# Performance work log

Hardware: AMD Instinct MI355X
Metric: run time of the kernel (lower is better)

Reference implementation:

```python
import jax, jax.numpy as jnp
import numpy as np

B, NT, NM, C, H, FF = 8, 1024, 2048, 1024, 8, 4096


def setup_inputs() -> dict:
    key = jax.random.key(0)
    ks = jax.random.split(key, 8)
    w = lambda k, shape, s=0.02: jax.random.normal(k, shape, dtype=jnp.float32) * s
    return {
        "tgt": jax.random.normal(ks[0], (B, NT, C), dtype=jnp.float32),
        "memory": jax.random.normal(ks[1], (B, NM, C), dtype=jnp.float32),
        "qkv_w": w(ks[2], (3 * C, C)), "qkv_b": jnp.zeros((3 * C,), jnp.float32),
        "sa_out_w": w(ks[3], (C, C)), "sa_out_b": jnp.zeros((C,), jnp.float32),
        "in_proj_w": w(ks[4], (3 * C, C)), "in_proj_b": jnp.zeros((3 * C,), jnp.float32),
        "mha_out_w": w(ks[5], (C, C)), "mha_out_b": jnp.zeros((C,), jnp.float32),
        "lin1_w": w(ks[6], (FF, C)), "lin1_b": jnp.zeros((FF,), jnp.float32),
        "lin2_w": w(ks[7], (C, FF)), "lin2_b": jnp.zeros((C,), jnp.float32),
        "ln1_g": jnp.ones((C,), jnp.float32), "ln1_b": jnp.zeros((C,), jnp.float32),
        "ln2_g": jnp.ones((C,), jnp.float32), "ln2_b": jnp.zeros((C,), jnp.float32),
        "ln3_g": jnp.ones((C,), jnp.float32), "ln3_b": jnp.zeros((C,), jnp.float32),
    }


def _ln(x, g, b):
    m = x.mean(-1, keepdims=True)
    v = jnp.mean((x - m) ** 2, axis=-1, keepdims=True)
    return (x - m) / jnp.sqrt(v + 1e-5) * g + b


def reference(tgt, memory, qkv_w, qkv_b, sa_out_w, sa_out_b,
              in_proj_w, in_proj_b, mha_out_w, mha_out_b,
              lin1_w, lin1_b, lin2_w, lin2_b,
              ln1_g, ln1_b, ln2_g, ln2_b, ln3_g, ln3_b):
    Bx, N, Cx = tgt.shape
    # ---- LocalSelfAttention: dense QK^T masked to diagonal-only window ----
    qkv = tgt @ qkv_w.T + qkv_b                      # [B,N,3C]
    q, k, v = jnp.split(qkv, 3, axis=-1)             # each [B,N,C]
    # NOTE: original multiplies by sqrt(embed_dim) (scale = sqrt, not 1/sqrt)
    scores = jnp.einsum('bnc,bmc->bnm', q, k) * jnp.sqrt(jnp.float32(Cx))
    diag = jnp.eye(N, dtype=bool)                    # registered diagonal mask
    scores = jnp.where(diag[None, :, :], scores, -jnp.inf)
    attn = jax.nn.softmax(scores, axis=-1)           # degenerates to identity
    sa = jnp.einsum('bnm,bmc->bnc', attn, v) @ sa_out_w.T + sa_out_b
    x = _ln(tgt + sa, ln1_g, ln1_b)
    # ---- cross multi-head attention over memory ----
    d = Cx // H
    wq, wk, wv = jnp.split(in_proj_w, 3, axis=0)
    bq, bk, bv = jnp.split(in_proj_b, 3, axis=0)
    qh = (x @ wq.T + bq).reshape(Bx, N, H, d).transpose(0, 2, 1, 3)       # [B,H,N,d]
    kh = (memory @ wk.T + bk).reshape(Bx, -1, H, d).transpose(0, 2, 1, 3)  # [B,H,M,d]
    vh = (memory @ wv.T + bv).reshape(Bx, -1, H, d).transpose(0, 2, 1, 3)
    a = jax.nn.softmax(jnp.einsum('bhnd,bhmd->bhnm', qh, kh) / jnp.sqrt(jnp.float32(d)), axis=-1)
    ca = jnp.einsum('bhnm,bhmd->bhnd', a, vh).transpose(0, 2, 1, 3).reshape(Bx, N, Cx)
    ca = ca @ mha_out_w.T + mha_out_b
    x = _ln(x + ca, ln2_g, ln2_b)
    # ---- FFN (relu) ----
    ff = jax.nn.relu(x @ lin1_w.T + lin1_b) @ lin2_w.T + lin2_b
    return _ln(x + ff, ln3_g, ln3_b)
```

## Files before the change

kernel.cpp:

```cpp
#include <hip/hip_runtime.h>
#include <hip/hip_bf16.h>
#include <cstddef>
#include <cstdint>

static constexpr int Cdim = 1024;
static constexpr int Bdim = 8;
static constexpr int NT   = 1024;
static constexpr int NM   = 2048;
static constexpr int Dh   = 128;
static constexpr int FF   = 4096;

typedef __attribute__((ext_vector_type(8))) short bf16x8_t;
typedef __attribute__((ext_vector_type(4))) float f32x4_t;

__device__ __forceinline__ float bf2f(unsigned int u16) {
    return __uint_as_float(u16 << 16);
}
__device__ __forceinline__ unsigned short f2bf(float f) {
    unsigned int u = __float_as_uint(f);
    u += 0x7fffu + ((u >> 16) & 1u);
    return (unsigned short)(u >> 16);
}

__device__ __forceinline__ void gload16(const void* g, void* l) {
    __builtin_amdgcn_global_load_lds(
        (const __attribute__((address_space(1))) void*)g,
        (__attribute__((address_space(3))) void*)l, 16, 0, 0);
}

__global__ __launch_bounds__(256)
void cvt_k(const float* __restrict__ in, unsigned short* __restrict__ out, int n8)
{
    const int stride = gridDim.x * 256;
    for (int i = blockIdx.x * 256 + threadIdx.x; i < n8; i += stride) {
        const float4 a = ((const float4*)in)[2*i];
        const float4 b = ((const float4*)in)[2*i+1];
        uint4 o;
        o.x = (unsigned)f2bf(a.x) | ((unsigned)f2bf(a.y) << 16);
        o.y = (unsigned)f2bf(a.z) | ((unsigned)f2bf(a.w) << 16);
        o.z = (unsigned)f2bf(b.x) | ((unsigned)f2bf(b.y) << 16);
        o.w = (unsigned)f2bf(b.z) | ((unsigned)f2bf(b.w) << 16);
        ((uint4*)out)[i] = o;
    }
}

template<int EPI, bool OBF>
__global__ __launch_bounds__(256)
void gemm_bf16_k(const unsigned short* __restrict__ A,
                 const unsigned short* __restrict__ W,
                 const float* __restrict__ bias, const float* __restrict__ resid,
                 void* __restrict__ outv, int Rows, int Cout, int K)
{
    __shared__ unsigned short As[128*32];
    __shared__ unsigned short Bs[128*32];
    const int gx  = gridDim.x;
    const int lin = blockIdx.y * gx + blockIdx.x;
    const int cpx = (gx * gridDim.y) >> 3;
    const int swz = (lin & 7) * cpx + (lin >> 3);
    const int bm = (swz / gx) * 128;
    const int bn = (swz % gx) * 128;
    const int t = threadIdx.x;
    const int w = t >> 6, l = t & 63;
    const int wr = w >> 1, wc = w & 1;

    f32x4_t acc[4][4];
    #pragma unroll
    for (int m = 0; m < 4; ++m)
        #pragma unroll
        for (int n = 0; n < 4; ++n) acc[m][n] = {0.f, 0.f, 0.f, 0.f};

    const int rA = 2*w*16 + (l >> 2);
    const int kc = (l & 3) * 8;
    const unsigned short* gA0 = A + (size_t)(bm + rA) * K + kc;
    const unsigned short* gA1 = gA0 + (size_t)16 * K;
    const unsigned short* gB0 = W + (size_t)(bn + rA) * K + kc;
    const unsigned short* gB1 = gB0 + (size_t)16 * K;
    unsigned short* lA0 = As + 2*w*512;
    unsigned short* lA1 = As + (2*w+1)*512;
    unsigned short* lB0 = Bs + 2*w*512;
    unsigned short* lB1 = Bs + (2*w+1)*512;

    const int frow = l & 15;
    const int kq   = l >> 4;
    const int abase = (wr*64 + frow)*64 + kq*16;
    const int bbase = (wc*64 + frow)*64 + kq*16;

    for (int k0 = 0; k0 < K; k0 += 32) {
        gload16(gA0, lA0); gload16(gA1, lA1);
        gload16(gB0, lB0); gload16(gB1, lB1);
        gA0 += 32; gA1 += 32; gB0 += 32; gB1 += 32;
        __syncthreads();
        bf16x8_t af[4], bfr[4];
        #pragma unroll
        for (int m = 0; m < 4; ++m)
            af[m] = *(const bf16x8_t*)((const char*)As + abase + m*1024);
        #pragma unroll
        for (int n = 0; n < 4; ++n)
            bfr[n] = *(const bf16x8_t*)((const char*)Bs + bbase + n*1024);
        #pragma unroll
        for (int m = 0; m < 4; ++m)
            #pragma unroll
            for (int n = 0; n < 4; ++n)
                acc[m][n] = __builtin_amdgcn_mfma_f32_16x16x32_bf16(
                                af[m], bfr[n], acc[m][n], 0, 0, 0);
        __syncthreads();
    }

    const int col0 = l & 15;
    const int r0   = (l >> 4) * 4;
    float bv[4];
    #pragma unroll
    for (int n = 0; n < 4; ++n) bv[n] = bias[bn + wc*64 + n*16 + col0];

    #pragma unroll
    for (int m = 0; m < 4; ++m)
        #pragma unroll
        for (int r = 0; r < 4; ++r) {
            const int row = bm + wr*64 + m*16 + r0 + r;
            #pragma unroll
            for (int n = 0; n < 4; ++n) {
                const int col = bn + wc*64 + n*16 + col0;
                const size_t idx = (size_t)row * Cout + col;
                float v = acc[m][n][r] + bv[n];
                if (EPI == 1) v += resid[idx];
                if (EPI == 2) v = fmaxf(v, 0.f);
                if (OBF) ((unsigned short*)outv)[idx] = f2bf(v);
                else     ((float*)outv)[idx] = v;
            }
        }
}

__global__ __launch_bounds__(256)
void vtrans_k(const unsigned short* __restrict__ kvb, unsigned short* __restrict__ vT)
{
    __shared__ unsigned short Ls[64][80];
    const int mt = blockIdx.x;
    const int ct = blockIdx.y;
    const int b  = blockIdx.z;
    const int t  = threadIdx.x;
    const int lr = t >> 3;
    const int cc = (t & 7) * 8;
    #pragma unroll
    for (int i = 0; i < 2; ++i) {
        const int m = lr + i*32;
        const uint4 v = *(const uint4*)(kvb +
            ((size_t)(b*NM + mt*64 + m))*(2*Cdim) + Cdim + ct*64 + cc);
        const unsigned short* s = (const unsigned short*)&v;
        #pragma unroll
        for (int j = 0; j < 8; ++j) {
            const int row = cc + j;
            Ls[row][8*((m >> 3) ^ (row >> 3)) + (m & 7)] = s[j];
        }
    }
    __syncthreads();
    #pragma unroll
    for (int i = 0; i < 2; ++i) {
        const int c  = lr + i*32;
        const int cg = ct*64 + c;
        const int h  = cg >> 7, dd = cg & 127;
        const uint4 v = *(const uint4*)&Ls[c][8*((t & 7) ^ (c >> 3))];
        *(uint4*)(vT + ((size_t)((b*8 + h)*128 + dd))*NM + mt*64 + cc) = v;
    }
}

__global__ __launch_bounds__(256)
void flash_attn_k(const unsigned short* __restrict__ qh,
                  const unsigned short* __restrict__ kvb,
                  const unsigned short* __restrict__ vT,
                  unsigned short* __restrict__ ca)
{
    __shared__ unsigned short Ks [64*128];
    __shared__ unsigned short VTs[128*64];
    __shared__ unsigned short Ps [64*64];

    const int lin = blockIdx.y * 16 + blockIdx.x;
    const int swz = (lin & 7) * 128 + (lin >> 3);
    const int qt = swz & 15;
    const int bh = swz >> 4;
    const int b = bh >> 3, h = bh & 7;
    const int t = threadIdx.x;
    const int w = t >> 6, l = t & 63;
    const float scale = 0.08838834764831845f;

    bf16x8_t aq[4];
    {
        const unsigned short* qbase = qh +
            ((size_t)(b*NT + qt*64 + w*16 + (l & 15)))*Cdim + h*Dh + (l >> 4)*8;
        #pragma unroll
        for (int kk = 0; kk < 4; ++kk)
            aq[kk] = *(const bf16x8_t*)(qbase + kk*32);
    }

    const unsigned short* ksrc[4];
    const unsigned short* vsrc[4];
    #pragma unroll
    for (int j = 0; j < 4; ++j) {
        const int chunk = 4*w + j;
        const int krow  = chunk*4 + (l >> 4);
        ksrc[j] = kvb + (size_t)(b*NM + krow)*(2*Cdim) + h*Dh
                      + (((l & 15) ^ (krow & 7)) * 8);
        const int dd = chunk*8 + (l >> 3);
        vsrc[j] = vT + (size_t)(bh*128 + dd)*NM + (((l & 7) ^ (dd & 7)) * 8);
    }
    unsigned short* kdst = Ks  + 4*w*512;
    unsigned short* vdst = VTs + 4*w*512;

    f32x4_t oacc[8];
    #pragma unroll
    for (int n = 0; n < 8; ++n) oacc[n] = {0.f, 0.f, 0.f, 0.f};
    float mrow[4] = {-1e30f, -1e30f, -1e30f, -1e30f};
    float lsum[4] = {0.f, 0.f, 0.f, 0.f};

    for (int m0 = 0; m0 < NM; m0 += 64) {
        __syncthreads();
        #pragma unroll
        for (int j = 0; j < 4; ++j) {
            gload16(ksrc[j] + (size_t)m0*(2*Cdim), kdst + j*512);
            gload16(vsrc[j] + m0,                  vdst + j*512);
        }
        __syncthreads();

        f32x4_t sacc[4];
        #pragma unroll
        for (int n = 0; n < 4; ++n) sacc[n] = {0.f, 0.f, 0.f, 0.f};
        #pragma unroll
        for (int n = 0; n < 4; ++n) {
            const int key = 16*n + (l & 15);
            #pragma unroll
            for (int kk = 0; kk < 4; ++kk) {
                const int slot = 4*kk + (l >> 4);
                const bf16x8_t bk = *(const bf16x8_t*)
                    (Ks + key*128 + ((slot ^ (key & 7)) * 8));
                sacc[n] = __builtin_amdgcn_mfma_f32_16x16x32_bf16(
                              aq[kk], bk, sacc[n], 0, 0, 0);
            }
        }

        #pragma unroll
        for (int r = 0; r < 4; ++r) {
            float s0 = sacc[0][r]*scale, s1 = sacc[1][r]*scale;
            float s2 = sacc[2][r]*scale, s3 = sacc[3][r]*scale;
            float cm = fmaxf(fmaxf(s0, s1), fmaxf(s2, s3));
            cm = fmaxf(cm, __shfl_xor(cm, 1, 16));
            cm = fmaxf(cm, __shfl_xor(cm, 2, 16));
            cm = fmaxf(cm, __shfl_xor(cm, 4, 16));
            cm = fmaxf(cm, __shfl_xor(cm, 8, 16));
            const float mnew = fmaxf(mrow[r], cm);
            const float corr = __expf(mrow[r] - mnew);
            mrow[r] = mnew;
            const float p0 = __expf(s0 - mnew), p1 = __expf(s1 - mnew);
            const float p2 = __expf(s2 - mnew), p3 = __expf(s3 - mnew);
            float rs = p0 + p1 + p2 + p3;
            rs += __shfl_xor(rs, 1, 16);
            rs += __shfl_xor(rs, 2, 16);
            rs += __shfl_xor(rs, 4, 16);
            rs += __shfl_xor(rs, 8, 16);
            lsum[r] = lsum[r]*corr + rs;
            #pragma unroll
            for (int n = 0; n < 8; ++n) oacc[n][r] *= corr;
            const int q = w*16 + (l >> 4)*4 + r;
            const float pv[4] = {p0, p1, p2, p3};
            #pragma unroll
            for (int n = 0; n < 4; ++n) {
                const int k = 16*n + (l & 15);
                Ps[q*64 + (((k >> 3) ^ (q & 7)) * 8) + (k & 7)] = f2bf(pv[n]);
            }
        }

        #pragma unroll
        for (int kk = 0; kk < 2; ++kk) {
            const int qa   = w*16 + (l & 15);
            const int slot = 4*kk + (l >> 4);
            const bf16x8_t pa = *(const bf16x8_t*)
                (Ps + qa*64 + ((slot ^ (qa & 7)) * 8));
            #pragma unroll
            for (int n = 0; n < 8; ++n) {
                const int dd = 16*n + (l & 15);
                const bf16x8_t bv = *(const bf16x8_t*)
                    (VTs + dd*64 + ((slot ^ (dd & 7)) * 8));
                oacc[n] = __builtin_amdgcn_mfma_f32_16x16x32_bf16(
                              pa, bv, oacc[n], 0, 0, 0);
            }
        }
    }

    #pragma unroll
    for (int r = 0; r < 4; ++r) {
        const float rinv = 1.0f / lsum[r];
        unsigned short* crow = ca +
            ((size_t)(b*NT + qt*64 + w*16 + (l >> 4)*4 + r))*Cdim + h*Dh + (l & 15);
        #pragma unroll
        for (int n = 0; n < 8; ++n)
            crow[16*n] = f2bf(oacc[n][r] * rinv);
    }
}

template<bool DUAL>
__global__ __launch_bounds__(256)
void ln_k(const float* __restrict__ in, const float* __restrict__ gam,
          const float* __restrict__ bet, float* __restrict__ out,
          unsigned short* __restrict__ out_bf)
{
    __shared__ float red[8];
    const int row = blockIdx.x;
    const int t = threadIdx.x;
    const float4 x = *(const float4*)(in + (size_t)row*Cdim + t*4);
    float s = x.x + x.y + x.z + x.w;
    #pragma unroll
    for (int m = 1; m < 64; m <<= 1) s += __shfl_xor(s, m, 64);
    if ((t & 63) == 0) red[t >> 6] = s;
    __syncthreads();
    const float mean = (red[0]+red[1]+red[2]+red[3]) * (1.0f/1024.0f);
    const float dx = x.x-mean, dy = x.y-mean, dz = x.z-mean, dw = x.w-mean;
    float q = dx*dx + dy*dy + dz*dz + dw*dw;
    #pragma unroll
    for (int m = 1; m < 64; m <<= 1) q += __shfl_xor(q, m, 64);
    if ((t & 63) == 0) red[4 + (t >> 6)] = q;
    __syncthreads();
    const float var = (red[4]+red[5]+red[6]+red[7]) * (1.0f/1024.0f);
    const float inv = 1.0f / sqrtf(var + 1e-5f);
    const float4 g  = *(const float4*)(gam + t*4);
    const float4 bb = *(const float4*)(bet + t*4);
    const float r0 = dx*inv*g.x+bb.x, r1 = dy*inv*g.y+bb.y;
    const float r2 = dz*inv*g.z+bb.z, r3 = dw*inv*g.w+bb.w;
    *(float4*)(out + (size_t)row*Cdim + t*4) = make_float4(r0,r1,r2,r3);
    if (DUAL) {
        uint2 pk;
        pk.x = (unsigned)f2bf(r0) | ((unsigned)f2bf(r1) << 16);
        pk.y = (unsigned)f2bf(r2) | ((unsigned)f2bf(r3) << 16);
        *(uint2*)(out_bf + (size_t)row*Cdim + t*4) = pk;
    }
}

extern "C" void kernel_launch(void* const* d_in, const int* in_sizes, int n_in,
                              void* d_out, int out_size, void* d_ws, size_t ws_size,
                              hipStream_t stream)
{
    const float* tgt      = (const float*)d_in[0];
    const float* memory   = (const float*)d_in[1];
    const float* qkv_w    = (const float*)d_in[2];
    const float* qkv_b    = (const float*)d_in[3];
    const float* sa_out_w = (const float*)d_in[4];
    const float* sa_out_b = (const float*)d_in[5];
    const float* in_w     = (const float*)d_in[6];
    const float* in_b     = (const float*)d_in[7];
    const float* mha_w    = (const float*)d_in[8];
    const float* mha_b    = (const float*)d_in[9];
    const float* lin1_w   = (const float*)d_in[10];
    const float* lin1_b   = (const float*)d_in[11];
    const float* lin2_w   = (const float*)d_in[12];
    const float* lin2_b   = (const float*)d_in[13];
    const float* ln1_g    = (const float*)d_in[14];
    const float* ln1_bb   = (const float*)d_in[15];
    const float* ln2_g    = (const float*)d_in[16];
    const float* ln2_bb   = (const float*)d_in[17];
    const float* ln3_g    = (const float*)d_in[18];
    const float* ln3_bb   = (const float*)d_in[19];

    const size_t MB = 1024*1024;
    if (ws_size < 220*MB) return;
    char* p = (char*)d_ws;
    unsigned short* wv   = (unsigned short*)p; p += 2*MB;
    unsigned short* wsa  = (unsigned short*)p; p += 2*MB;
    unsigned short* win  = (unsigned short*)p; p += 6*MB;
    unsigned short* wmh  = (unsigned short*)p; p += 2*MB;
    unsigned short* wl1  = (unsigned short*)p; p += 8*MB;
    unsigned short* wl2  = (unsigned short*)p; p += 8*MB;
    float* resb = (float*)p; p += 32*MB;
    float* x12  = (float*)p; p += 32*MB;
    unsigned short* kvff = (unsigned short*)p; p += 64*MB;
    unsigned short* vq   = (unsigned short*)p; p += 16*MB;
    unsigned short* regG = (unsigned short*)p; p += 16*MB;
    unsigned short* regH = (unsigned short*)p; p += 32*MB;
    unsigned short* vT   = (unsigned short*)resb;
    unsigned short* tgtb = regG;
    unsigned short* x1b  = regG;
    unsigned short* memb = regH;
    unsigned short* cabf = regH;
    unsigned short* x2b  = (unsigned short*)((char*)regH + 16*MB);
    float* x1 = x12;
    float* x2 = x12;

    const int R  = Bdim * NT;
    const int RM = Bdim * NM;
    dim3 blk(256);
    auto cvgrid = [](int n8){ int b = (n8 + 255) / 256; return dim3(b > 2048 ? 2048 : b); };

    cvt_k<<<cvgrid(R*Cdim/8),      blk, 0, stream>>>(tgt,                 tgtb, R*Cdim/8);
    cvt_k<<<cvgrid(RM*Cdim/8),     blk, 0, stream>>>(memory,              memb, RM*Cdim/8);
    cvt_k<<<cvgrid(Cdim*Cdim/8),   blk, 0, stream>>>(qkv_w + 2*Cdim*Cdim, wv,   Cdim*Cdim/8);
    cvt_k<<<cvgrid(Cdim*Cdim/8),   blk, 0, stream>>>(sa_out_w,            wsa,  Cdim*Cdim/8);
    cvt_k<<<cvgrid(3*Cdim*Cdim/8), blk, 0, stream>>>(in_w,                win,  3*Cdim*Cdim/8);
    cvt_k<<<cvgrid(Cdim*Cdim/8),   blk, 0, stream>>>(mha_w,               wmh,  Cdim*Cdim/8);
    cvt_k<<<cvgrid(FF*Cdim/8),     blk, 0, stream>>>(lin1_w,              wl1,  FF*Cdim/8);
    cvt_k<<<cvgrid(FF*Cdim/8),     blk, 0, stream>>>(lin2_w,              wl2,  FF*Cdim/8);

    gemm_bf16_k<0,true ><<<dim3( 8,  64), blk, 0, stream>>>(tgtb, wv,  qkv_b + 2*Cdim, nullptr, vq,   R,  Cdim,   Cdim);
    gemm_bf16_k<1,false><<<dim3( 8,  64), blk, 0, stream>>>(vq,   wsa, sa_out_b,       tgt,     resb, R,  Cdim,   Cdim);
    ln_k<true ><<<dim3(R), blk, 0, stream>>>(resb, ln1_g, ln1_bb, x1, x1b);
    gemm_bf16_k<0,true ><<<dim3( 8,  64), blk, 0, stream>>>(x1b,  win, in_b,           nullptr, vq,   R,  Cdim,   Cdim);
    gemm_bf16_k<0,true ><<<dim3(16, 128), blk, 0, stream>>>(memb, win + Cdim*Cdim, in_b + Cdim, nullptr, kvff, RM, 2*Cdim, Cdim);
    vtrans_k<<<dim3(32, 16, 8), blk, 0, stream>>>(kvff, vT);
    flash_attn_k<<<dim3(16, 64), blk, 0, stream>>>(vq, kvff, vT, cabf);
    gemm_bf16_k<1,false><<<dim3( 8,  64), blk, 0, stream>>>(cabf, wmh, mha_b,          x1,      resb, R,  Cdim,   Cdim);
    ln_k<true ><<<dim3(R), blk, 0, stream>>>(resb, ln2_g, ln2_bb, x2, x2b);
    gemm_bf16_k<2,true ><<<dim3(32,  64), blk, 0, stream>>>(x2b,  wl1, lin1_b,         nullptr, kvff, R,  FF,     Cdim);
    gemm_bf16_k<1,false><<<dim3( 8,  64), blk, 0, stream>>>(kvff, wl2, lin2_b,         x2,      resb, R,  Cdim,   FF);
    ln_k<false><<<dim3(R), blk, 0, stream>>>(resb, ln3_g, ln3_bb, (float*)d_out, nullptr);
}
```

Baseline: 866.1 us.

## Double-buffer flash attention K/V loads, fuse conversions, wave-per-row layernorm

Flash attention now prefetches the next K/V tile into a second LDS buffer while computing on the current one, using explicit vmcnt waits, and raises wave priority around the MFMA sections. The eight fp32-to-bf16 conversion launches are merged into one kernel that picks its segment by block index. Layernorm is reorganized so each wavefront handles one row, dropping the shared-memory reduction and block barriers. Doubling LDS use in attention may lower occupancy.

```diff
diff --git a/kernel.cpp b/kernel.cpp
--- a/kernel.cpp
+++ b/kernel.cpp
@@ -28,20 +28,29 @@
         (__attribute__((address_space(3))) void*)l, 16, 0, 0);
 }
 
+struct CvtArgs {
+    const float* src[8];
+    unsigned short* dst[8];
+};
+
 __global__ __launch_bounds__(256)
-void cvt_k(const float* __restrict__ in, unsigned short* __restrict__ out, int n8)
-{
-    const int stride = gridDim.x * 256;
-    for (int i = blockIdx.x * 256 + threadIdx.x; i < n8; i += stride) {
-        const float4 a = ((const float4*)in)[2*i];
-        const float4 b = ((const float4*)in)[2*i+1];
-        uint4 o;
-        o.x = (unsigned)f2bf(a.x) | ((unsigned)f2bf(a.y) << 16);
-        o.y = (unsigned)f2bf(a.z) | ((unsigned)f2bf(a.w) << 16);
-        o.z = (unsigned)f2bf(b.x) | ((unsigned)f2bf(b.y) << 16);
-        o.w = (unsigned)f2bf(b.z) | ((unsigned)f2bf(b.w) << 16);
-        ((uint4*)out)[i] = o;
-    }
+void cvt_all_k(CvtArgs a)
+{
+    constexpr int cum[8] = {0, 8, 24, 25, 26, 29, 30, 34};
+    const int u = blockIdx.x >> 9;
+    int seg = 0;
+    #pragma unroll
+    for (int s = 1; s < 8; ++s) seg = (u >= cum[s]) ? s : seg;
+    const size_t i8 = (size_t)(blockIdx.x - (cum[seg] << 9)) * 256 + threadIdx.x;
+    const float* sp = a.src[seg] + i8 * 8;
+    const float4 x = ((const float4*)sp)[0];
+    const float4 y = ((const float4*)sp)[1];
+    uint4 o;
+    o.x = (unsigned)f2bf(x.x) | ((unsigned)f2bf(x.y) << 16);
+    o.y = (unsigned)f2bf(x.z) | ((unsigned)f2bf(x.w) << 16);
+    o.z = (unsigned)f2bf(y.x) | ((unsigned)f2bf(y.y) << 16);
+    o.w = (unsigned)f2bf(y.z) | ((unsigned)f2bf(y.w) << 16);
+    *(uint4*)(a.dst[seg] + i8 * 8) = o;
 }
 
 template<int EPI, bool OBF>
@@ -169,8 +178,8 @@
                   const unsigned short* __restrict__ vT,
                   unsigned short* __restrict__ ca)
 {
-    __shared__ unsigned short Ks [64*128];
-    __shared__ unsigned short VTs[128*64];
+    __shared__ unsigned short Ks [2][64*128];
+    __shared__ unsigned short VTs[2][128*64];
     __shared__ unsigned short Ps [64*64];
 
     const int lin = blockIdx.y * 16 + blockIdx.x;
@@ -202,8 +211,6 @@
         const int dd = chunk*8 + (l >> 3);
         vsrc[j] = vT + (size_t)(bh*128 + dd)*NM + (((l & 7) ^ (dd & 7)) * 8);
     }
-    unsigned short* kdst = Ks  + 4*w*512;
-    unsigned short* vdst = VTs + 4*w*512;
 
     f32x4_t oacc[8];
     #pragma unroll
@@ -211,18 +218,33 @@
     float mrow[4] = {-1e30f, -1e30f, -1e30f, -1e30f};
     float lsum[4] = {0.f, 0.f, 0.f, 0.f};
 
-    for (int m0 = 0; m0 < NM; m0 += 64) {
-        __syncthreads();
-        #pragma unroll
-        for (int j = 0; j < 4; ++j) {
-            gload16(ksrc[j] + (size_t)m0*(2*Cdim), kdst + j*512);
-            gload16(vsrc[j] + m0,                  vdst + j*512);
-        }
-        __syncthreads();
+    #pragma unroll
+    for (int j = 0; j < 4; ++j) {
+        gload16(ksrc[j], &Ks[0][4*w*512 + j*512]);
+        gload16(vsrc[j], &VTs[0][4*w*512 + j*512]);
+    }
+
+    for (int tt = 0; tt < 32; ++tt) {
+        const int buf = tt & 1;
+        if (tt < 31) {
+            const size_t koff = (size_t)((tt + 1) * 64) * (2*Cdim);
+            const int    moff = (tt + 1) * 64;
+            #pragma unroll
+            for (int j = 0; j < 4; ++j) {
+                gload16(ksrc[j] + koff, &Ks[buf ^ 1][4*w*512 + j*512]);
+                gload16(vsrc[j] + moff, &VTs[buf ^ 1][4*w*512 + j*512]);
+            }
+            asm volatile("s_waitcnt vmcnt(8)" ::: "memory");
+        } else {
+            asm volatile("s_waitcnt vmcnt(0)" ::: "memory");
+        }
+        __builtin_amdgcn_sched_barrier(0);
+        __builtin_amdgcn_s_barrier();
 
         f32x4_t sacc[4];
         #pragma unroll
         for (int n = 0; n < 4; ++n) sacc[n] = {0.f, 0.f, 0.f, 0.f};
+        __builtin_amdgcn_s_setprio(1);
         #pragma unroll
         for (int n = 0; n < 4; ++n) {
             const int key = 16*n + (l & 15);
@@ -230,11 +252,12 @@
             for (int kk = 0; kk < 4; ++kk) {
                 const int slot = 4*kk + (l >> 4);
                 const bf16x8_t bk = *(const bf16x8_t*)
-                    (Ks + key*128 + ((slot ^ (key & 7)) * 8));
+                    (&Ks[buf][key*128 + ((slot ^ (key & 7)) * 8)]);
                 sacc[n] = __builtin_amdgcn_mfma_f32_16x16x32_bf16(
                               aq[kk], bk, sacc[n], 0, 0, 0);
             }
         }
+        __builtin_amdgcn_s_setprio(0);
 
         #pragma unroll
         for (int r = 0; r < 4; ++r) {
@@ -267,6 +290,7 @@
             }
         }
 
+        __builtin_amdgcn_s_setprio(1);
         #pragma unroll
         for (int kk = 0; kk < 2; ++kk) {
             const int qa   = w*16 + (l & 15);
@@ -277,11 +301,15 @@
             for (int n = 0; n < 8; ++n) {
                 const int dd = 16*n + (l & 15);
                 const bf16x8_t bv = *(const bf16x8_t*)
-                    (VTs + dd*64 + ((slot ^ (dd & 7)) * 8));
+                    (&VTs[buf][dd*64 + ((slot ^ (dd & 7)) * 8)]);
                 oacc[n] = __builtin_amdgcn_mfma_f32_16x16x32_bf16(
                               pa, bv, oacc[n], 0, 0, 0);
             }
         }
+        __builtin_amdgcn_s_setprio(0);
+
+        __builtin_amdgcn_sched_barrier(0);
+        __builtin_amdgcn_s_barrier();
     }
 
     #pragma unroll
@@ -301,34 +329,43 @@
           const float* __restrict__ bet, float* __restrict__ out,
           unsigned short* __restrict__ out_bf)
 {
-    __shared__ float red[8];
-    const int row = blockIdx.x;
-    const int t = threadIdx.x;
-    const float4 x = *(const float4*)(in + (size_t)row*Cdim + t*4);
-    float s = x.x + x.y + x.z + x.w;
+    const int row = blockIdx.x*4 + (threadIdx.x >> 6);
+    const int l   = threadIdx.x & 63;
+    const float* rp = in + (size_t)row*Cdim;
+    float4 x[4];
+    #pragma unroll
+    for (int j = 0; j < 4; ++j) x[j] = *(const float4*)(rp + j*256 + l*4);
+    float s = 0.f;
+    #pragma unroll
+    for (int j = 0; j < 4; ++j) s += x[j].x + x[j].y + x[j].z + x[j].w;
     #pragma unroll
     for (int m = 1; m < 64; m <<= 1) s += __shfl_xor(s, m, 64);
-    if ((t & 63) == 0) red[t >> 6] = s;
-    __syncthreads();
-    const float mean = (red[0]+red[1]+red[2]+red[3]) * (1.0f/1024.0f);
-    const float dx = x.x-mean, dy = x.y-mean, dz = x.z-mean, dw = x.w-mean;
-    float q = dx*dx + dy*dy + dz*dz + dw*dw;
+    const float mean = s * (1.0f/1024.0f);
+    float q = 0.f;
+    #pragma unroll
+    for (int j = 0; j < 4; ++j) {
+        const float dx = x[j].x-mean, dy = x[j].y-mean;
+        const float dz = x[j].z-mean, dw = x[j].w-mean;
+        q += dx*dx + dy*dy + dz*dz + dw*dw;
+    }
     #pragma unroll
     for (int m = 1; m < 64; m <<= 1) q += __shfl_xor(q, m, 64);
-    if ((t & 63) == 0) red[4 + (t >> 6)] = q;
-    __syncthreads();
-    const float var = (red[4]+red[5]+red[6]+red[7]) * (1.0f/1024.0f);
-    const float inv = 1.0f / sqrtf(var + 1e-5f);
-    const float4 g  = *(const float4*)(gam + t*4);
-    const float4 bb = *(const float4*)(bet + t*4);
-    const float r0 = dx*inv*g.x+bb.x, r1 = dy*inv*g.y+bb.y;
-    const float r2 = dz*inv*g.z+bb.z, r3 = dw*inv*g.w+bb.w;
-    *(float4*)(out + (size_t)row*Cdim + t*4) = make_float4(r0,r1,r2,r3);
-    if (DUAL) {
-        uint2 pk;
-        pk.x = (unsigned)f2bf(r0) | ((unsigned)f2bf(r1) << 16);
-        pk.y = (unsigned)f2bf(r2) | ((unsigned)f2bf(r3) << 16);
-        *(uint2*)(out_bf + (size_t)row*Cdim + t*4) = pk;
+    const float inv = 1.0f / sqrtf(q * (1.0f/1024.0f) + 1e-5f);
+    #pragma unroll
+    for (int j = 0; j < 4; ++j) {
+        const float4 g  = *(const float4*)(gam + j*256 + l*4);
+        const float4 bb = *(const float4*)(bet + j*256 + l*4);
+        const float r0 = (x[j].x-mean)*inv*g.x + bb.x;
+        const float r1 = (x[j].y-mean)*inv*g.y + bb.y;
+        const float r2 = (x[j].z-mean)*inv*g.z + bb.z;
+        const float r3 = (x[j].w-mean)*inv*g.w + bb.w;
+        *(float4*)(out + (size_t)row*Cdim + j*256 + l*4) = make_float4(r0,r1,r2,r3);
+        if (DUAL) {
+            uint2 pk;
+            pk.x = (unsigned)f2bf(r0) | ((unsigned)f2bf(r1) << 16);
+            pk.y = (unsigned)f2bf(r2) | ((unsigned)f2bf(r3) << 16);
+            *(uint2*)(out_bf + (size_t)row*Cdim + j*256 + l*4) = pk;
+        }
     }
 }
 
@@ -384,27 +421,28 @@
     const int R  = Bdim * NT;
     const int RM = Bdim * NM;
     dim3 blk(256);
-    auto cvgrid = [](int n8){ int b = (n8 + 255) / 256; return dim3(b > 2048 ? 2048 : b); };
-
-    cvt_k<<<cvgrid(R*Cdim/8),      blk, 0, stream>>>(tgt,                 tgtb, R*Cdim/8);
-    cvt_k<<<cvgrid(RM*Cdim/8),     blk, 0, stream>>>(memory,              memb, RM*Cdim/8);
-    cvt_k<<<cvgrid(Cdim*Cdim/8),   blk, 0, stream>>>(qkv_w + 2*Cdim*Cdim, wv,   Cdim*Cdim/8);
-    cvt_k<<<cvgrid(Cdim*Cdim/8),   blk, 0, stream>>>(sa_out_w,            wsa,  Cdim*Cdim/8);
-    cvt_k<<<cvgrid(3*Cdim*Cdim/8), blk, 0, stream>>>(in_w,                win,  3*Cdim*Cdim/8);
-    cvt_k<<<cvgrid(Cdim*Cdim/8),   blk, 0, stream>>>(mha_w,               wmh,  Cdim*Cdim/8);
-    cvt_k<<<cvgrid(FF*Cdim/8),     blk, 0, stream>>>(lin1_w,              wl1,  FF*Cdim/8);
-    cvt_k<<<cvgrid(FF*Cdim/8),     blk, 0, stream>>>(lin2_w,              wl2,  FF*Cdim/8);
+
+    CvtArgs cva;
+    cva.src[0] = tgt;                  cva.dst[0] = tgtb;
+    cva.src[1] = memory;               cva.dst[1] = memb;
+    cva.src[2] = qkv_w + 2*Cdim*Cdim;  cva.dst[2] = wv;
+    cva.src[3] = sa_out_w;             cva.dst[3] = wsa;
+    cva.src[4] = in_w;                 cva.dst[4] = win;
+    cva.src[5] = mha_w;                cva.dst[5] = wmh;
+    cva.src[6] = lin1_w;               cva.dst[6] = wl1;
+    cva.src[7] = lin2_w;               cva.dst[7] = wl2;
+    cvt_all_k<<<dim3(38*512), blk, 0, stream>>>(cva);
 
     gemm_bf16_k<0,true ><<<dim3( 8,  64), blk, 0, stream>>>(tgtb, wv,  qkv_b + 2*Cdim, nullptr, vq,   R,  Cdim,   Cdim);
     gemm_bf16_k<1,false><<<dim3( 8,  64), blk, 0, stream>>>(vq,   wsa, sa_out_b,       tgt,     resb, R,  Cdim,   Cdim);
-    ln_k<true ><<<dim3(R), blk, 0, stream>>>(resb, ln1_g, ln1_bb, x1, x1b);
+    ln_k<true ><<<dim3(R/4), blk, 0, stream>>>(resb, ln1_g, ln1_bb, x1, x1b);
     gemm_bf16_k<0,true ><<<dim3( 8,  64), blk, 0, stream>>>(x1b,  win, in_b,           nullptr, vq,   R,  Cdim,   Cdim);
     gemm_bf16_k<0,true ><<<dim3(16, 128), blk, 0, stream>>>(memb, win + Cdim*Cdim, in_b + Cdim, nullptr, kvff, RM, 2*Cdim, Cdim);
     vtrans_k<<<dim3(32, 16, 8), blk, 0, stream>>>(kvff, vT);
     flash_attn_k<<<dim3(16, 64), blk, 0, stream>>>(vq, kvff, vT, cabf);
     gemm_bf16_k<1,false><<<dim3( 8,  64), blk, 0, stream>>>(cabf, wmh, mha_b,          x1,      resb, R,  Cdim,   Cdim);
-    ln_k<true ><<<dim3(R), blk, 0, stream>>>(resb, ln2_g, ln2_bb, x2, x2b);
+    ln_k<true ><<<dim3(R/4), blk, 0, stream>>>(resb, ln2_g, ln2_bb, x2, x2b);
     gemm_bf16_k<2,true ><<<dim3(32,  64), blk, 0, stream>>>(x2b,  wl1, lin1_b,         nullptr, kvff, R,  FF,     Cdim);
     gemm_bf16_k<1,false><<<dim3( 8,  64), blk, 0, stream>>>(kvff, wl2, lin2_b,         x2,      resb, R,  Cdim,   FF);
-    ln_k<false><<<dim3(R), blk, 0, stream>>>(resb, ln3_g, ln3_bb, (float*)d_out, nullptr);
-}
+    ln_k<false><<<dim3(R/4), blk, 0, stream>>>(resb, ln3_g, ln3_bb, (float*)d_out, nullptr);
+}
```

Measured after the change: 838.3 us. 3.2% less time.
